# Kernel tuning notes

Hardware: AMD Instinct MI355X
Metric: run time of the kernel (lower is better)

Reference implementation:

```python
import jax, jax.numpy as jnp
import numpy as np

B, S, H = 2, 2048, 1024
NH, KVH, HD = 16, 4, 64
EPS = 1e-6


def setup_inputs() -> dict:
    key = jax.random.key(0)
    ks = jax.random.split(key, 6)
    hidden_states = jax.random.normal(ks[0], (B, S, H), jnp.float32)
    # additive causal mask [B,1,S,S]
    neg = jnp.finfo(jnp.float32).min
    causal = jnp.where(jnp.tril(jnp.ones((S, S), bool)), 0.0, neg)
    attention_mask = jnp.broadcast_to(causal[None, None], (B, 1, S, S))
    # RoPE cos/sin [B,S,HD]
    pos = jnp.arange(S, dtype=jnp.float32)
    inv_freq = 1.0 / (10000.0 ** (jnp.arange(0, HD, 2, dtype=jnp.float32) / HD))
    freqs = pos[:, None] * inv_freq[None, :]          # [S, HD//2]
    emb = jnp.concatenate([freqs, freqs], axis=-1)    # [S, HD]
    cos = jnp.broadcast_to(jnp.cos(emb)[None], (B, S, HD))
    sin = jnp.broadcast_to(jnp.sin(emb)[None], (B, S, HD))
    scale = 0.02
    q_weight = jax.random.normal(ks[1], (NH * HD, H), jnp.float32) * scale
    k_weight = jax.random.normal(ks[2], (KVH * HD, H), jnp.float32) * scale
    v_weight = jax.random.normal(ks[3], (KVH * HD, H), jnp.float32) * scale
    o_weight = jax.random.normal(ks[4], (H, NH * HD), jnp.float32) * scale
    q_norm_weight = jnp.ones((HD,), jnp.float32)
    k_norm_weight = jnp.ones((HD,), jnp.float32)
    return dict(hidden_states=hidden_states, attention_mask=attention_mask,
                cos=cos, sin=sin, q_weight=q_weight, k_weight=k_weight,
                v_weight=v_weight, o_weight=o_weight,
                q_norm_weight=q_norm_weight, k_norm_weight=k_norm_weight)


def _rotate_half(x):
    x1, x2 = x[..., : x.shape[-1] // 2], x[..., x.shape[-1] // 2:]
    return jnp.concatenate([-x2, x1], axis=-1)


def _rms_norm(x, w, eps=EPS):
    xf = x.astype(jnp.float32)
    var = jnp.mean(xf * xf, axis=-1, keepdims=True)
    return (w * (xf * jax.lax.rsqrt(var + eps)).astype(x.dtype))


def reference(hidden_states, attention_mask, cos, sin, q_weight, k_weight,
              v_weight, o_weight, q_norm_weight, k_norm_weight):
    b, s, h = hidden_states.shape
    # projections (torch F.linear: x @ W.T)
    q = (hidden_states @ q_weight.T).reshape(b, s, NH, HD).transpose(0, 2, 1, 3)
    k = (hidden_states @ k_weight.T).reshape(b, s, KVH, HD).transpose(0, 2, 1, 3)
    v = (hidden_states @ v_weight.T).reshape(b, s, KVH, HD).transpose(0, 2, 1, 3)
    # per-head QK RMSNorm (Qwen3 style)
    q = _rms_norm(q, q_norm_weight)
    k = _rms_norm(k, k_norm_weight)
    # RoPE, cos/sin broadcast over head axis
    c, si = cos[:, None], sin[:, None]                 # [B,1,S,HD]
    q = q * c + _rotate_half(q) * si
    k = k * c + _rotate_half(k) * si
    # GQA: repeat kv heads
    rep = NH // KVH
    k = jnp.repeat(k, rep, axis=1)
    v = jnp.repeat(v, rep, axis=1)
    # attention
    scores = jnp.einsum('bhqd,bhkd->bhqk', q, k) * (HD ** -0.5)
    scores = scores + attention_mask[:, :, :, :s]
    attn = jax.nn.softmax(scores.astype(jnp.float32), axis=-1).astype(q.dtype)
    out = jnp.einsum('bhqk,bhkd->bhqd', attn, v)
    out = out.transpose(0, 2, 1, 3).reshape(b, s, NH * HD)
    return out @ o_weight.T
```

## Files before the change

### kernel.cpp

```cpp
#include <hip/hip_runtime.h>

typedef unsigned short u16;
typedef __attribute__((ext_vector_type(4))) float f32x4;
typedef __attribute__((ext_vector_type(8))) __bf16 bf16x8;
typedef __attribute__((ext_vector_type(8))) unsigned short u16x8;
typedef __attribute__((ext_vector_type(4))) unsigned short u16x4;

#define NEGINF -3.0e38f

#define BB 2
#define SS 2048
#define HH 1024
#define NHEAD 16
#define KVHEAD 4
#define HD 64
#define BS (BB*SS)
#define NQKV 1536

#define QSCALE 0.18033688f
#define SMBIAS -11.5415603f

__device__ __forceinline__ u16 f2bf(float f) {
  union { float f; unsigned int u; } v; v.f = f;
  unsigned int r = v.u + 0x7FFFu + ((v.u >> 16) & 1u);
  return (u16)(r >> 16);
}
__device__ __forceinline__ float bf2f(u16 h) {
  union { unsigned int u; float f; } v; v.u = ((unsigned int)h) << 16;
  return v.f;
}

typedef const unsigned int __attribute__((address_space(1)))* gp_t;
typedef unsigned int __attribute__((address_space(3)))* lp_t;
__device__ __forceinline__ void gload_lds16(const void* g, void* l) {
  __builtin_amdgcn_global_load_lds((gp_t)g, (lp_t)l, 16, 0, 0);
}

__global__ __launch_bounds__(256) void cvt_all(
    const float* __restrict__ h, const float* __restrict__ qw,
    const float* __restrict__ kw, const float* __restrict__ vw,
    const float* __restrict__ ow,
    u16* __restrict__ Xb, u16* __restrict__ Wqkv, u16* __restrict__ Wo) {
  long i = ((long)blockIdx.x * 256 + threadIdx.x) * 4;
  const float* src; u16* dst;
  if (i < 4194304L)      { src = h  + i;             dst = Xb   + i; }
  else if (i < 5242880L) { src = qw + (i - 4194304); dst = Wqkv + (i - 4194304); }
  else if (i < 5505024L) { src = kw + (i - 5242880); dst = Wqkv + (i - 4194304); }
  else if (i < 5767168L) { src = vw + (i - 5505024); dst = Wqkv + (i - 4194304); }
  else                   { src = ow + (i - 5767168); dst = Wo   + (i - 5767168); }
  float4 v = *(const float4*)src;
  u16x4 o;
  o.x = f2bf(v.x); o.y = f2bf(v.y); o.z = f2bf(v.z); o.w = f2bf(v.w);
  *(u16x4*)dst = o;
}

template<int EPI>
__global__ __launch_bounds__(256) void gemm_bt(
    const u16* __restrict__ A, const u16* __restrict__ Bw,
    float* __restrict__ Cf,
    u16* __restrict__ Qb, u16* __restrict__ Kb, u16* __restrict__ Vb,
    const float* __restrict__ cosb, const float* __restrict__ sinb,
    const float* __restrict__ qnw, const float* __restrict__ knw,
    int M, int N, int K)
{
  __shared__ u16 As[2][64 * 64];
  __shared__ u16 Bs[2][128 * 64];
  const int tid = threadIdx.x;
  const int w = tid >> 6, l = tid & 63;
  const int lg = l >> 4, lc = l & 15;
  const int m0 = blockIdx.y * 64, n0 = blockIdx.x * 128;
  const int wr = (w >> 1) * 32, wc = (w & 1) * 64;

  const f32x4 vzero = {0.f, 0.f, 0.f, 0.f};
  f32x4 acc[2][4];
#pragma unroll
  for (int i = 0; i < 2; ++i)
#pragma unroll
    for (int j = 0; j < 4; ++j) acc[i][j] = vzero;

  const u16* Ap = A + (size_t)m0 * K;
  const u16* Bp = Bw + (size_t)n0 * K;
  const int nk = K >> 6;

  const int arow = tid >> 3, ach = tid & 7;

#define GSTAGE(bufi, kt)                                                         \
  {                                                                              \
    _Pragma("unroll") for (int c = 0; c < 2; ++c) {                              \
      int row = c * 32 + arow;                                                   \
      gload_lds16(Ap + (size_t)row * K + (kt) * 64 + (ach ^ (row & 7)) * 8,      \
                  (char*)As[bufi] + c * 4096 + w * 1024);                        \
    }                                                                            \
    _Pragma("unroll") for (int c = 0; c < 4; ++c) {                              \
      int row = c * 32 + arow;                                                   \
      gload_lds16(Bp + (size_t)row * K + (kt) * 64 + (ach ^ (row & 7)) * 8,      \
                  (char*)Bs[bufi] + c * 4096 + w * 1024);                        \
    }                                                                            \
  }

  GSTAGE(0, 0)
  __syncthreads();

  for (int kt = 0; kt < nk; ++kt) {
    const int cur = kt & 1;
    if (kt + 1 < nk) GSTAGE(cur ^ 1, kt + 1)

    bf16x8 af[2][2], bfr[4][2];
#pragma unroll
    for (int i = 0; i < 2; ++i) {
      int row = wr + i * 16 + lc;
#pragma unroll
      for (int c = 0; c < 2; ++c)
        af[i][c] = *(const bf16x8*)&As[cur][row * 64 + (((c * 4 + lg) ^ (lc & 7)) << 3)];
    }
#pragma unroll
    for (int i = 0; i < 4; ++i) {
      int row = wc + i * 16 + lc;
#pragma unroll
      for (int c = 0; c < 2; ++c)
        bfr[i][c] = *(const bf16x8*)&Bs[cur][row * 64 + (((c * 4 + lg) ^ (lc & 7)) << 3)];
    }
    __builtin_amdgcn_s_setprio(1);
#pragma unroll
    for (int c = 0; c < 2; ++c)
#pragma unroll
      for (int am = 0; am < 2; ++am)
#pragma unroll
        for (int bn = 0; bn < 4; ++bn)
          acc[am][bn] = __builtin_amdgcn_mfma_f32_16x16x32_bf16(af[am][c], bfr[bn][c], acc[am][bn], 0, 0, 0);
    __builtin_amdgcn_s_setprio(0);

    if (kt + 1 < nk) __syncthreads();
  }
#undef GSTAGE

  if (EPI == 1) {
#pragma unroll
    for (int am = 0; am < 2; ++am)
#pragma unroll
      for (int bn = 0; bn < 4; ++bn)
#pragma unroll
        for (int r = 0; r < 4; ++r) {
          int m = m0 + wr + am * 16 + lg * 4 + r;
          int n = n0 + wc + bn * 16 + lc;
          Cf[(size_t)m * N + n] = acc[am][bn][r];
        }
  } else {
    const int nb = n0 + wc;
    if (nb < 1280) {
      const bool isQ = (nb < 1024);
      const int head = isQ ? (nb >> 6) : ((nb - 1024) >> 6);
      u16* dst = isQ ? (Qb + ((size_t)head * SS) * HD)
                     : (Kb + ((size_t)head * SS) * HD);
      const size_t hstride = (size_t)(isQ ? NHEAD : KVHEAD) * SS * HD;
      const float* wt = isQ ? qnw : knw;
      const float posc = isQ ? QSCALE : 1.0f;
      float wt4[4];
#pragma unroll
      for (int bn = 0; bn < 4; ++bn) wt4[bn] = wt[bn * 16 + lc];
#pragma unroll
      for (int am = 0; am < 2; ++am)
#pragma unroll
        for (int r = 0; r < 4; ++r) {
          int m = m0 + wr + am * 16 + lg * 4 + r;
          int bb = m >> 11, s2 = m & 2047;
          float ss = 0.f;
#pragma unroll
          for (int bn = 0; bn < 4; ++bn) ss += acc[am][bn][r] * acc[am][bn][r];
          ss += __shfl_xor(ss, 1);
          ss += __shfl_xor(ss, 2);
          ss += __shfl_xor(ss, 4);
          ss += __shfl_xor(ss, 8);
          float rs = rsqrtf(ss * (1.0f / 64.0f) + 1e-6f);
          size_t cbase = ((size_t)bb * SS + s2) * HD;
          size_t obase = bb * hstride + (size_t)s2 * HD;
#pragma unroll
          for (int bn = 0; bn < 4; ++bn) {
            int d = bn * 16 + lc;
            float xn = acc[am][bn][r] * rs * wt4[bn];
            float xp = acc[am][bn ^ 2][r] * rs * wt4[bn ^ 2];
            float rot = (bn < 2) ? -xp : xp;
            float o = (xn * cosb[cbase + d] + rot * sinb[cbase + d]) * posc;
            dst[obase + d] = f2bf(o);
          }
        }
    } else {
      const int kh = (nb - 1280) >> 6;
#pragma unroll
      for (int am = 0; am < 2; ++am)
#pragma unroll
        for (int r = 0; r < 4; ++r) {
          int m = m0 + wr + am * 16 + lg * 4 + r;
          int bb = m >> 11, s2 = m & 2047;
#pragma unroll
          for (int bn = 0; bn < 4; ++bn) {
            int d = bn * 16 + lc;
            Vb[(((size_t)bb * KVHEAD + kh) * HD + d) * SS + s2] = f2bf(acc[am][bn][r]);
          }
        }
    }
  }
}

__global__ __launch_bounds__(256) void attn_kernel(
    const u16* __restrict__ Qb, const u16* __restrict__ Kb,
    const u16* __restrict__ Vt, u16* __restrict__ Ob)
{
  __shared__ u16 Ks[3][64 * 64];
  __shared__ u16 Vs[3][64 * 64];

  const int tid = threadIdx.x;
  const int w = tid >> 6, l = tid & 63;
  const int lg = l >> 4, lc = l & 15;

  const int bid = blockIdx.x;
  const int a = bid & 7, hb = (bid >> 3) & 31, hi = bid >> 8;
  const int qt = hi ? (15 - a) : a;
  const int h = hb & 15, b = hb >> 4;
  const int q0 = qt * 128;
  const int kvh = h >> 2;

  const u16* Qp = Qb + (((size_t)b * NHEAD + h) * SS + q0 + w * 32) * HD;
  const u16* Kp = Kb + ((size_t)b * KVHEAD + kvh) * SS * HD;
  const u16* Vp = Vt + ((size_t)b * KVHEAD + kvh) * (size_t)HD * SS;

  bf16x8 qa[2][2];
#pragma unroll
  for (int qf = 0; qf < 2; ++qf)
#pragma unroll
    for (int c = 0; c < 2; ++c)
      qa[qf][c] = *(const bf16x8*)(Qp + (qf * 16 + lc) * HD + c * 32 + lg * 8);

  const f32x4 vzero = {0.f, 0.f, 0.f, 0.f};
  const f32x4 zbias = {SMBIAS, SMBIAS, SMBIAS, SMBIAS};
  f32x4 acc[2][4];
  float lsum[2] = {0.f, 0.f};
#pragma unroll
  for (int qf = 0; qf < 2; ++qf)
#pragma unroll
    for (int df = 0; df < 4; ++df) acc[qf][df] = vzero;

  const int srow0 = w * 8 + (l >> 3);
  const int srow1 = srow0 + 32;
  const int sswz = (l >> 3) ^ ((w & 1) << 2);
  const int ss0 = (l & 7) ^ sswz;
  const int nt = 2 * qt + 2;

  int ko[8], vo[8];
#pragma unroll
  for (int f = 0; f < 4; ++f) {
    int row = ((lc >> 2) << 3) + ((f & 1) << 2) + (lc & 3) + ((f >> 1) << 5);
    int swz = (((f & 1) << 2) + (lc & 3)) ^ (((lc >> 2) & 1) << 2);
    ko[2 * f]     = row * 64 + ((lg ^ swz) << 3);
    ko[2 * f + 1] = row * 64 + (((4 + lg) ^ swz) << 3);
  }
#pragma unroll
  for (int df = 0; df < 4; ++df) {
    int vrow = 16 * df + lc;
    int vswz = (lc & 7) ^ (((lc >> 3) & 1) << 2);
    vo[2 * df]     = vrow * 64 + ((lg ^ vswz) << 3);
    vo[2 * df + 1] = vrow * 64 + (((4 + lg) ^ vswz) << 3);
  }

#define STAGE(bufi, kvbase)                                                          \
  gload_lds16(Kp + (size_t)((kvbase) + srow0) * HD + ss0 * 8, (char*)Ks[bufi] + w * 1024);        \
  gload_lds16(Kp + (size_t)((kvbase) + srow1) * HD + ss0 * 8, (char*)Ks[bufi] + 4096 + w * 1024); \
  gload_lds16(Vp + (size_t)srow0 * SS + (kvbase) + ss0 * 8, (char*)Vs[bufi] + w * 1024);          \
  gload_lds16(Vp + (size_t)srow1 * SS + (kvbase) + ss0 * 8, (char*)Vs[bufi] + 4096 + w * 1024);

  STAGE(0, 0)
  STAGE(1, 64)
  __syncthreads();

  int rd = 0;
  for (int kt = 0; kt < nt; ++kt) {
    int st = rd + 2; if (st >= 3) st -= 3;
    if (kt + 2 < nt) { STAGE(st, (kt + 2) * 64) }

    const int kv0 = kt * 64;
    if (kv0 <= q0 + w * 32 + 31) {
      const u16* KsB = Ks[rd];
      const u16* VsB = Vs[rd];

      bf16x8 kb[8], vb[8];
#pragma unroll
      for (int i = 0; i < 8; ++i) kb[i] = *(const bf16x8*)&KsB[ko[i]];
#pragma unroll
      for (int i = 0; i < 8; ++i) vb[i] = *(const bf16x8*)&VsB[vo[i]];

      const bool diag = (kv0 + 63 > q0 + w * 32);
      bf16x8 pa[2][2];
#pragma unroll
      for (int c = 0; c < 2; ++c) {
        f32x4 sv[2][2];
#pragma unroll
        for (int fs = 0; fs < 2; ++fs) {
          const int f = 2 * c + fs;
#pragma unroll
          for (int qf = 0; qf < 2; ++qf) {
            f32x4 z = zbias;
            z = __builtin_amdgcn_mfma_f32_16x16x32_bf16(kb[2 * f], qa[qf][0], z, 0, 0, 0);
            z = __builtin_amdgcn_mfma_f32_16x16x32_bf16(kb[2 * f + 1], qa[qf][1], z, 0, 0, 0);
            sv[qf][fs] = z;
          }
        }
        if (diag) {
          const int keyb = kv0 + c * 32 + lg * 8;
#pragma unroll
          for (int qf = 0; qf < 2; ++qf) {
            const int qi = q0 + w * 32 + qf * 16 + lc;
#pragma unroll
            for (int fs = 0; fs < 2; ++fs)
#pragma unroll
              for (int rr = 0; rr < 4; ++rr) {
                int key = keyb + fs * 4 + rr;
                if (key > qi) sv[qf][fs][rr] = NEGINF;
              }
          }
        }
#pragma unroll
        for (int qf = 0; qf < 2; ++qf) {
#pragma unroll
          for (int fs = 0; fs < 2; ++fs)
#pragma unroll
            for (int rr = 0; rr < 4; ++rr) {
              float p = __builtin_amdgcn_exp2f(sv[qf][fs][rr]);
              sv[qf][fs][rr] = p;
              lsum[qf] += p;
            }
#pragma unroll
          for (int j = 0; j < 8; ++j)
            pa[qf][c][j] = (__bf16)sv[qf][j >> 2][j & 3];
        }
      }

#pragma unroll
      for (int df = 0; df < 4; ++df)
#pragma unroll
        for (int qf = 0; qf < 2; ++qf) {
          acc[qf][df] = __builtin_amdgcn_mfma_f32_16x16x32_bf16(pa[qf][0], vb[2 * df], acc[qf][df], 0, 0, 0);
          acc[qf][df] = __builtin_amdgcn_mfma_f32_16x16x32_bf16(pa[qf][1], vb[2 * df + 1], acc[qf][df], 0, 0, 0);
        }
    }

    if (kt + 1 < nt) __syncthreads();
    rd = (rd + 1 == 3) ? 0 : rd + 1;
  }
#undef STAGE

#pragma unroll
  for (int qf = 0; qf < 2; ++qf) {
    float t = lsum[qf];
    t += __shfl_xor(t, 16);
    t += __shfl_xor(t, 32);
#pragma unroll
    for (int r = 0; r < 4; ++r) {
      float dnm = __shfl(t, lg * 4 + r);
      float inv = 1.0f / dnm;
      int qi = q0 + w * 32 + qf * 16 + lg * 4 + r;
#pragma unroll
      for (int df = 0; df < 4; ++df)
        Ob[((size_t)b * SS + qi) * (NHEAD * HD) + h * HD + df * 16 + lc] =
            f2bf(acc[qf][df][r] * inv);
    }
  }
}

extern "C" void kernel_launch(void* const* d_in, const int* in_sizes, int n_in,
                              void* d_out, int out_size, void* d_ws, size_t ws_size,
                              hipStream_t stream) {
  const float* hidden = (const float*)d_in[0];
  const float* cosb = (const float*)d_in[2];
  const float* sinb = (const float*)d_in[3];
  const float* qw = (const float*)d_in[4];
  const float* kw = (const float*)d_in[5];
  const float* vw = (const float*)d_in[6];
  const float* ow = (const float*)d_in[7];
  const float* qnw = (const float*)d_in[8];
  const float* knw = (const float*)d_in[9];
  float* out = (float*)d_out;

  u16* Xb   = (u16*)d_ws;
  u16* Wqkv = Xb + (size_t)BS * HH;
  u16* Wo   = Wqkv + (size_t)NQKV * HH;
  u16* Qb   = Wo + (size_t)HH * HH;
  u16* Kb   = Qb + (size_t)BB * NHEAD * SS * HD;
  u16* Vb   = Kb + (size_t)BB * KVHEAD * SS * HD;
  u16* Ab   = Vb + (size_t)BB * KVHEAD * SS * HD;

  cvt_all<<<6656, 256, 0, stream>>>(hidden, qw, kw, vw, ow, Xb, Wqkv, Wo);

  gemm_bt<0><<<dim3(NQKV / 128, BS / 64), 256, 0, stream>>>(
      Xb, Wqkv, nullptr, Qb, Kb, Vb, cosb, sinb, qnw, knw, BS, NQKV, HH);

  attn_kernel<<<512, 256, 0, stream>>>(Qb, Kb, Vb, Ab);

  gemm_bt<1><<<dim3(HH / 128, BS / 64), 256, 0, stream>>>(
      Ab, Wo, out, nullptr, nullptr, nullptr, nullptr, nullptr, nullptr, nullptr, BS, HH, HH);
}
```

Measured before the change: 90.49 us.

## Balance causal attention work with split-KV pairing and a combine kernel

Each block pair now covers a short and a long query tile. Block half 0 finishes the short tile and processes the first KV segment of the long tile, and block half 1 processes the remainder, so both blocks get equal tile counts. Partial unnormalized accumulators and row sums are written to a float workspace, and a new combine kernel sums them and normalizes. The pipeline also drops from triple to double buffering of the K/V tiles. The cost is an extra kernel launch, extra global traffic for the partials, and more syncs per tile.

```diff
diff --git a/kernel.cpp b/kernel.cpp
--- a/kernel.cpp
+++ b/kernel.cpp
@@ -19,6 +19,8 @@
 
 #define QSCALE 0.18033688f
 #define SMBIAS -11.5415603f
+
+#define PSLOT 8320
 
 __device__ __forceinline__ u16 f2bf(float f) {
   union { float f; unsigned int u; } v; v.f = f;
@@ -204,32 +206,26 @@
 
 __global__ __launch_bounds__(256) void attn_kernel(
     const u16* __restrict__ Qb, const u16* __restrict__ Kb,
-    const u16* __restrict__ Vt, u16* __restrict__ Ob)
+    const u16* __restrict__ Vt, u16* __restrict__ Ob,
+    float* __restrict__ Pw)
 {
-  __shared__ u16 Ks[3][64 * 64];
-  __shared__ u16 Vs[3][64 * 64];
+  __shared__ u16 Ks[2][64 * 64];
+  __shared__ u16 Vs[2][64 * 64];
 
   const int tid = threadIdx.x;
   const int w = tid >> 6, l = tid & 63;
   const int lg = l >> 4, lc = l & 15;
 
   const int bid = blockIdx.x;
-  const int a = bid & 7, hb = (bid >> 3) & 31, hi = bid >> 8;
-  const int qt = hi ? (15 - a) : a;
+  const int p = bid & 255, half = bid >> 8;
+  const int qt_s = p & 7, hb = p >> 3;
   const int h = hb & 15, b = hb >> 4;
-  const int q0 = qt * 128;
+  const int qt_l = 15 - qt_s;
+  const int L1 = 2 * qt_s + 2;
   const int kvh = h >> 2;
 
-  const u16* Qp = Qb + (((size_t)b * NHEAD + h) * SS + q0 + w * 32) * HD;
   const u16* Kp = Kb + ((size_t)b * KVHEAD + kvh) * SS * HD;
   const u16* Vp = Vt + ((size_t)b * KVHEAD + kvh) * (size_t)HD * SS;
-
-  bf16x8 qa[2][2];
-#pragma unroll
-  for (int qf = 0; qf < 2; ++qf)
-#pragma unroll
-    for (int c = 0; c < 2; ++c)
-      qa[qf][c] = *(const bf16x8*)(Qp + (qf * 16 + lc) * HD + c * 32 + lg * 8);
 
   const f32x4 vzero = {0.f, 0.f, 0.f, 0.f};
   const f32x4 zbias = {SMBIAS, SMBIAS, SMBIAS, SMBIAS};
@@ -244,7 +240,6 @@
   const int srow1 = srow0 + 32;
   const int sswz = (l >> 3) ^ ((w & 1) << 2);
   const int ss0 = (l & 7) ^ sswz;
-  const int nt = 2 * qt + 2;
 
   int ko[8], vo[8];
 #pragma unroll
@@ -268,101 +263,158 @@
   gload_lds16(Vp + (size_t)srow0 * SS + (kvbase) + ss0 * 8, (char*)Vs[bufi] + w * 1024);          \
   gload_lds16(Vp + (size_t)srow1 * SS + (kvbase) + ss0 * 8, (char*)Vs[bufi] + 4096 + w * 1024);
 
-  STAGE(0, 0)
-  STAGE(1, 64)
-  __syncthreads();
-
-  int rd = 0;
-  for (int kt = 0; kt < nt; ++kt) {
-    int st = rd + 2; if (st >= 3) st -= 3;
-    if (kt + 2 < nt) { STAGE(st, (kt + 2) * 64) }
-
-    const int kv0 = kt * 64;
-    if (kv0 <= q0 + w * 32 + 31) {
-      const u16* KsB = Ks[rd];
-      const u16* VsB = Vs[rd];
-
-      bf16x8 kb[8], vb[8];
-#pragma unroll
-      for (int i = 0; i < 8; ++i) kb[i] = *(const bf16x8*)&KsB[ko[i]];
-#pragma unroll
-      for (int i = 0; i < 8; ++i) vb[i] = *(const bf16x8*)&VsB[vo[i]];
-
-      const bool diag = (kv0 + 63 > q0 + w * 32);
-      bf16x8 pa[2][2];
-#pragma unroll
-      for (int c = 0; c < 2; ++c) {
-        f32x4 sv[2][2];
-#pragma unroll
-        for (int fs = 0; fs < 2; ++fs) {
-          const int f = 2 * c + fs;
+  auto seg = [&](int qt, int lo, int hi, bool fin) {
+    const int q0 = qt * 128;
+    const u16* Qp = Qb + (((size_t)b * NHEAD + h) * SS + q0 + w * 32) * HD;
+    bf16x8 qa[2][2];
+#pragma unroll
+    for (int qf = 0; qf < 2; ++qf)
+#pragma unroll
+      for (int c = 0; c < 2; ++c)
+        qa[qf][c] = *(const bf16x8*)(Qp + (qf * 16 + lc) * HD + c * 32 + lg * 8);
+
+    STAGE(0, lo * 64)
+    __syncthreads();
+
+    for (int t = lo; t < hi; ++t) {
+      const int cur = (t - lo) & 1;
+      if (t + 1 < hi) { STAGE(cur ^ 1, (t + 1) * 64) }
+
+      const int kv0 = t * 64;
+      if (kv0 <= q0 + w * 32 + 31) {
+        const u16* KsB = Ks[cur];
+        const u16* VsB = Vs[cur];
+
+        bf16x8 kb[8], vb[8];
+#pragma unroll
+        for (int i = 0; i < 8; ++i) kb[i] = *(const bf16x8*)&KsB[ko[i]];
+#pragma unroll
+        for (int i = 0; i < 8; ++i) vb[i] = *(const bf16x8*)&VsB[vo[i]];
+
+        const bool diag = (kv0 + 63 > q0 + w * 32);
+        bf16x8 pa[2][2];
+#pragma unroll
+        for (int c = 0; c < 2; ++c) {
+          f32x4 sv[2][2];
+#pragma unroll
+          for (int fs = 0; fs < 2; ++fs) {
+            const int f = 2 * c + fs;
+#pragma unroll
+            for (int qf = 0; qf < 2; ++qf) {
+              f32x4 z = zbias;
+              z = __builtin_amdgcn_mfma_f32_16x16x32_bf16(kb[2 * f], qa[qf][0], z, 0, 0, 0);
+              z = __builtin_amdgcn_mfma_f32_16x16x32_bf16(kb[2 * f + 1], qa[qf][1], z, 0, 0, 0);
+              sv[qf][fs] = z;
+            }
+          }
+          if (diag) {
+            const int keyb = kv0 + c * 32 + lg * 8;
+#pragma unroll
+            for (int qf = 0; qf < 2; ++qf) {
+              const int qi = q0 + w * 32 + qf * 16 + lc;
+#pragma unroll
+              for (int fs = 0; fs < 2; ++fs)
+#pragma unroll
+                for (int rr = 0; rr < 4; ++rr) {
+                  int key = keyb + fs * 4 + rr;
+                  if (key > qi) sv[qf][fs][rr] = NEGINF;
+                }
+            }
+          }
 #pragma unroll
           for (int qf = 0; qf < 2; ++qf) {
-            f32x4 z = zbias;
-            z = __builtin_amdgcn_mfma_f32_16x16x32_bf16(kb[2 * f], qa[qf][0], z, 0, 0, 0);
-            z = __builtin_amdgcn_mfma_f32_16x16x32_bf16(kb[2 * f + 1], qa[qf][1], z, 0, 0, 0);
-            sv[qf][fs] = z;
+#pragma unroll
+            for (int fs = 0; fs < 2; ++fs)
+#pragma unroll
+              for (int rr = 0; rr < 4; ++rr) {
+                float pp = __builtin_amdgcn_exp2f(sv[qf][fs][rr]);
+                sv[qf][fs][rr] = pp;
+                lsum[qf] += pp;
+              }
+#pragma unroll
+            for (int j = 0; j < 8; ++j)
+              pa[qf][c][j] = (__bf16)sv[qf][j >> 2][j & 3];
           }
         }
-        if (diag) {
-          const int keyb = kv0 + c * 32 + lg * 8;
+
+#pragma unroll
+        for (int df = 0; df < 4; ++df)
 #pragma unroll
           for (int qf = 0; qf < 2; ++qf) {
-            const int qi = q0 + w * 32 + qf * 16 + lc;
-#pragma unroll
-            for (int fs = 0; fs < 2; ++fs)
-#pragma unroll
-              for (int rr = 0; rr < 4; ++rr) {
-                int key = keyb + fs * 4 + rr;
-                if (key > qi) sv[qf][fs][rr] = NEGINF;
-              }
-          }
+            acc[qf][df] = __builtin_amdgcn_mfma_f32_16x16x32_bf16(pa[qf][0], vb[2 * df], acc[qf][df], 0, 0, 0);
+            acc[qf][df] = __builtin_amdgcn_mfma_f32_16x16x32_bf16(pa[qf][1], vb[2 * df + 1], acc[qf][df], 0, 0, 0);
+          }
+      }
+
+      __syncthreads();
+    }
+
+    if (fin) {
+#pragma unroll
+      for (int qf = 0; qf < 2; ++qf) {
+        float t = lsum[qf];
+        t += __shfl_xor(t, 16);
+        t += __shfl_xor(t, 32);
+#pragma unroll
+        for (int rr = 0; rr < 4; ++rr) {
+          float dnm = __shfl(t, lg * 4 + rr);
+          float inv = 1.0f / dnm;
+          int qi = q0 + w * 32 + qf * 16 + lg * 4 + rr;
+#pragma unroll
+          for (int df = 0; df < 4; ++df)
+            Ob[((size_t)b * SS + qi) * (NHEAD * HD) + h * HD + df * 16 + lc] =
+                f2bf(acc[qf][df][rr] * inv);
         }
-#pragma unroll
-        for (int qf = 0; qf < 2; ++qf) {
-#pragma unroll
-          for (int fs = 0; fs < 2; ++fs)
-#pragma unroll
-            for (int rr = 0; rr < 4; ++rr) {
-              float p = __builtin_amdgcn_exp2f(sv[qf][fs][rr]);
-              sv[qf][fs][rr] = p;
-              lsum[qf] += p;
-            }
-#pragma unroll
-          for (int j = 0; j < 8; ++j)
-            pa[qf][c][j] = (__bf16)sv[qf][j >> 2][j & 3];
-        }
+        lsum[qf] = 0.f;
+#pragma unroll
+        for (int df = 0; df < 4; ++df) acc[qf][df] = vzero;
       }
-
+    }
+  };
+
+  if (half == 0) {
+    seg(qt_s, 0, L1, true);
+    seg(qt_l, 0, 17 - L1, false);
+  } else {
+    seg(qt_l, 17 - L1, 2 * qt_l + 2, false);
+  }
+#undef STAGE
+
+  float* slot = Pw + (size_t)(p * 2 + half) * PSLOT;
+#pragma unroll
+  for (int qf = 0; qf < 2; ++qf) {
+#pragma unroll
+    for (int rr = 0; rr < 4; ++rr) {
+      int row = w * 32 + qf * 16 + lg * 4 + rr;
 #pragma unroll
       for (int df = 0; df < 4; ++df)
-#pragma unroll
-        for (int qf = 0; qf < 2; ++qf) {
-          acc[qf][df] = __builtin_amdgcn_mfma_f32_16x16x32_bf16(pa[qf][0], vb[2 * df], acc[qf][df], 0, 0, 0);
-          acc[qf][df] = __builtin_amdgcn_mfma_f32_16x16x32_bf16(pa[qf][1], vb[2 * df + 1], acc[qf][df], 0, 0, 0);
-        }
-    }
-
-    if (kt + 1 < nt) __syncthreads();
-    rd = (rd + 1 == 3) ? 0 : rd + 1;
-  }
-#undef STAGE
-
-#pragma unroll
-  for (int qf = 0; qf < 2; ++qf) {
+        slot[row * 64 + df * 16 + lc] = acc[qf][df][rr];
+    }
     float t = lsum[qf];
     t += __shfl_xor(t, 16);
     t += __shfl_xor(t, 32);
-#pragma unroll
-    for (int r = 0; r < 4; ++r) {
-      float dnm = __shfl(t, lg * 4 + r);
-      float inv = 1.0f / dnm;
-      int qi = q0 + w * 32 + qf * 16 + lg * 4 + r;
-#pragma unroll
-      for (int df = 0; df < 4; ++df)
-        Ob[((size_t)b * SS + qi) * (NHEAD * HD) + h * HD + df * 16 + lc] =
-            f2bf(acc[qf][df][r] * inv);
-    }
+    if (l < 16) slot[8192 + w * 32 + qf * 16 + l] = t;
+  }
+}
+
+__global__ __launch_bounds__(256) void attn_combine(
+    const float* __restrict__ Pw, u16* __restrict__ Ob)
+{
+  const int blk = blockIdx.x;
+  const int p = blk >> 1, rh = blk & 1;
+  const int qt_s = p & 7, hb = p >> 3;
+  const int h = hb & 15, b = hb >> 4;
+  const int qt_l = 15 - qt_s;
+  const float* A = Pw + (size_t)(p * 2 + 0) * PSLOT;
+  const float* Bp = Pw + (size_t)(p * 2 + 1) * PSLOT;
+#pragma unroll
+  for (int i = 0; i < 16; ++i) {
+    int e = i * 256 + threadIdx.x;
+    int row = rh * 64 + (e >> 6), d = e & 63;
+    float s = A[row * 64 + d] + Bp[row * 64 + d];
+    float dn = A[8192 + row] + Bp[8192 + row];
+    int qrow = qt_l * 128 + row;
+    Ob[((size_t)b * SS + qrow) * (NHEAD * HD) + h * HD + d] = f2bf(s / dn);
   }
 }
 
@@ -387,13 +439,15 @@
   u16* Kb   = Qb + (size_t)BB * NHEAD * SS * HD;
   u16* Vb   = Kb + (size_t)BB * KVHEAD * SS * HD;
   u16* Ab   = Vb + (size_t)BB * KVHEAD * SS * HD;
+  float* Pw = (float*)(Ab + (size_t)BS * HH);
 
   cvt_all<<<6656, 256, 0, stream>>>(hidden, qw, kw, vw, ow, Xb, Wqkv, Wo);
 
   gemm_bt<0><<<dim3(NQKV / 128, BS / 64), 256, 0, stream>>>(
       Xb, Wqkv, nullptr, Qb, Kb, Vb, cosb, sinb, qnw, knw, BS, NQKV, HH);
 
-  attn_kernel<<<512, 256, 0, stream>>>(Qb, Kb, Vb, Ab);
+  attn_kernel<<<512, 256, 0, stream>>>(Qb, Kb, Vb, Ab, Pw);
+  attn_combine<<<512, 256, 0, stream>>>(Pw, Ab);
 
   gemm_bt<1><<<dim3(HH / 128, BS / 64), 256, 0, stream>>>(
       Ab, Wo, out, nullptr, nullptr, nullptr, nullptr, nullptr, nullptr, nullptr, BS, HH, HH);
```

Measured after the change: 85.58 us. 5.4% less time.
